# Performance work log

Hardware: AMD Instinct MI355X
Metric: run time of the kernel (lower is better)

The kernel has to match this reference:

```python
import jax, jax.numpy as jnp
import numpy as np

N_POINTS = 16384
N_GAUSS = 3200
N_CLASSES = 14
BOX = 10.0  # scene half-extent


def setup_inputs() -> dict:
    key = jax.random.key(0)
    ks = jax.random.split(key, 6)
    xyz = jax.random.uniform(ks[0], (N_POINTS, 3), jnp.float32, -BOX, BOX)
    means = jax.random.uniform(ks[1], (N_GAUSS, 3), jnp.float32, -BOX, BOX)
    scales = jax.random.uniform(ks[2], (N_GAUSS, 3), jnp.float32, 0.5, 2.0)
    rotations = jax.random.normal(ks[3], (N_GAUSS, 4), jnp.float32)
    opacities = jax.random.uniform(ks[4], (N_GAUSS,), jnp.float32, 0.1, 1.0)
    semantics = jax.random.normal(ks[5], (N_GAUSS, N_CLASSES), jnp.float32)
    return {"xyz": xyz, "means": means, "scales": scales,
            "rotations": rotations, "opacities": opacities, "semantics": semantics}


def quat_to_rot(q):
    # q: [G,4] in (w, x, y, z) order, normalized first (matches torch helper)
    q = q / jnp.linalg.norm(q, axis=-1, keepdims=True)
    w, x, y, z = q[:, 0], q[:, 1], q[:, 2], q[:, 3]
    R = jnp.stack([
        1 - 2 * (y * y + z * z), 2 * (x * y - w * z),     2 * (x * z + w * y),
        2 * (x * y + w * z),     1 - 2 * (x * x + z * z), 2 * (y * z - w * x),
        2 * (x * z - w * y),     2 * (y * z + w * x),     1 - 2 * (x * x + y * y),
    ], axis=-1).reshape(-1, 3, 3)
    return R


def reference(xyz, means, scales, rotations, opacities, semantics):
    # Cov = (S R)^T (S R) = R^T diag(s^2) R ; closed-form inverse (R orthonormal):
    # CovInv = R^T diag(1/s^2) R  -- fused analytic 3x3 inverse.
    R = quat_to_rot(rotations)                      # [G,3,3]
    inv_var = 1.0 / (scales * scales)               # [G,3]
    CovInv = jnp.einsum('gki,gk,gkj->gij', R, inv_var, R)  # [G,3,3]

    # Quadratic form q[n,g] = (x_n - mu_g)^T A_g (x_n - mu_g), expanded so that
    # only [N,G] is materialized (no [N,G,3] intermediates):
    Amu = jnp.einsum('gij,gj->gi', CovInv, means)   # [G,3]
    muAmu = jnp.sum(means * Amu, axis=-1)           # [G]
    P = (xyz[:, :, None] * xyz[:, None, :]).reshape(-1, 9)   # [N,9]
    Aflat = CovInv.reshape(-1, 9)                   # [G,9]
    q = P @ Aflat.T - 2.0 * (xyz @ Amu.T) + muAmu[None, :]   # [N,G]

    # Gaussian splat aggregation: semantics weighted by opacity * Gaussian kernel
    w = opacities[None, :] * jnp.exp(-0.5 * q)      # [N,G]
    out = w @ semantics                              # [N,C]
    return out
```

## Files before the change

### kernel.cpp

```cpp
#include <hip/hip_runtime.h>
#include <hip/hip_bf16.h>

#define N_POINTS 16384
#define N_GAUSS  3200
#define N_CLASSES 14
#define NCHUNK (N_GAUSS / 32)

typedef _Float16 half8  __attribute__((ext_vector_type(8)));
typedef _Float16 half2v __attribute__((ext_vector_type(2)));
typedef float    f32x4  __attribute__((ext_vector_type(4)));

#define WS_CREC_OFF 0
#define WS_SEMP_OFF 204800

__global__ void gauss_prep_kernel(const float* __restrict__ means,
                                  const float* __restrict__ scales,
                                  const float* __restrict__ rotations,
                                  const float* __restrict__ opacities,
                                  const float* __restrict__ semantics,
                                  _Float16* __restrict__ crec,
                                  _Float16* __restrict__ semP,
                                  float* __restrict__ out) {
    const int gid = blockIdx.x * blockDim.x + threadIdx.x;

#pragma unroll
    for (int i = 0; i < N_CLASSES; ++i)
        out[i * N_POINTS + gid] = 0.0f;

    const int g = gid;
    if (g >= N_GAUSS) return;

    float qw = rotations[g * 4 + 0];
    float qx = rotations[g * 4 + 1];
    float qy = rotations[g * 4 + 2];
    float qz = rotations[g * 4 + 3];
    float inv = 1.0f / sqrtf(qw * qw + qx * qx + qy * qy + qz * qz);
    qw *= inv; qx *= inv; qy *= inv; qz *= inv;

    float r00 = 1.0f - 2.0f * (qy * qy + qz * qz);
    float r01 = 2.0f * (qx * qy - qw * qz);
    float r02 = 2.0f * (qx * qz + qw * qy);
    float r10 = 2.0f * (qx * qy + qw * qz);
    float r11 = 1.0f - 2.0f * (qx * qx + qz * qz);
    float r12 = 2.0f * (qy * qz - qw * qx);
    float r20 = 2.0f * (qx * qz - qw * qy);
    float r21 = 2.0f * (qy * qz + qw * qx);
    float r22 = 1.0f - 2.0f * (qx * qx + qy * qy);

    float sx = scales[g * 3 + 0];
    float sy = scales[g * 3 + 1];
    float sz = scales[g * 3 + 2];
    float iv0 = 1.0f / (sx * sx);
    float iv1 = 1.0f / (sy * sy);
    float iv2 = 1.0f / (sz * sz);

    float a00 = iv0 * r00 * r00 + iv1 * r10 * r10 + iv2 * r20 * r20;
    float a01 = iv0 * r00 * r01 + iv1 * r10 * r11 + iv2 * r20 * r21;
    float a02 = iv0 * r00 * r02 + iv1 * r10 * r12 + iv2 * r20 * r22;
    float a11 = iv0 * r01 * r01 + iv1 * r11 * r11 + iv2 * r21 * r21;
    float a12 = iv0 * r01 * r02 + iv1 * r11 * r12 + iv2 * r21 * r22;
    float a22 = iv0 * r02 * r02 + iv1 * r12 * r12 + iv2 * r22 * r22;

    float mx = means[g * 3 + 0];
    float my = means[g * 3 + 1];
    float mz = means[g * 3 + 2];
    float amx = a00 * mx + a01 * my + a02 * mz;
    float amy = a01 * mx + a11 * my + a12 * mz;
    float amz = a02 * mx + a12 * my + a22 * mz;
    float muAmu = mx * amx + my * amy + mz * amz;

    const float k = -0.72134752044448170368f;

    float C[10];
    C[0] = k * a00;  C[1] = k * a11;  C[2] = k * a22;
    C[3] = 2.0f * k * a01;  C[4] = 2.0f * k * a02;  C[5] = 2.0f * k * a12;
    C[6] = -2.0f * k * amx; C[7] = -2.0f * k * amy; C[8] = -2.0f * k * amz;
    C[9] = k * muAmu + log2f(opacities[g]);

    _Float16* rec = crec + (size_t)g * 32;
#pragma unroll
    for (int kk = 0; kk < 10; ++kk) {
        _Float16 h = (_Float16)C[kk];
        rec[kk]      = h;
        rec[10 + kk] = (_Float16)(C[kk] - (float)h);
        rec[20 + kk] = h;
    }
    rec[30] = (_Float16)0; rec[31] = (_Float16)0;

    const int cidx = g >> 5, r = g & 31;
    const int gt = r >> 4, grpW = (r >> 2) & 3, i = r & 3;
    const int p = grpW * 8 + gt * 4 + i;
#pragma unroll
    for (int c = 0; c < N_CLASSES; ++c)
        semP[(size_t)c * N_GAUSS + cidx * 32 + p] = (_Float16)semantics[g * N_CLASSES + c];
}

__launch_bounds__(512, 4)
__global__ void gauss_occ_main_kernel(const float* __restrict__ xyz,
                                      const _Float16* __restrict__ crec,
                                      const _Float16* __restrict__ semP,
                                      float* __restrict__ out) {
    __shared__ unsigned int wbuf[8][64][16];

    const int tid  = threadIdx.x;
    const int lane = tid & 63;
    const int wid  = __builtin_amdgcn_readfirstlane(tid >> 6);
    const int pg    = blockIdx.x >> 2;
    const int split = blockIdx.x & 3;
    const int slot  = split * 8 + wid;
    const int c0 = (slot * NCHUNK) >> 5;
    const int c1 = ((slot + 1) * NCHUNK) >> 5;

    const int m   = lane & 15;
    const int mm  = (m < N_CLASSES) ? m : (N_CLASSES - 1);
    const int grp = lane >> 4;
    const int frs = (m >> 1) & 3;
    const int wsz = (lane >> 1) & 3;

    const int pt = pg * 64 + lane;
    const float x = xyz[pt * 3 + 0];
    const float y = xyz[pt * 3 + 1];
    const float z = xyz[pt * 3 + 2];

    unsigned int (*wrow)[16] = wbuf[wid];

    {
        float P[10] = {x * x, y * y, z * z, x * y, x * z, y * z, x, y, z, 1.0f};
        _Float16 Ph[10], Pl[10];
#pragma unroll
        for (int j = 0; j < 10; ++j) {
            Ph[j] = (_Float16)P[j];
            Pl[j] = (_Float16)(P[j] - (float)Ph[j]);
        }
        half8 b0, b1, b2, b3;
#pragma unroll
        for (int j = 0; j < 8; ++j) b0[j] = Ph[j];
        b1[0] = Ph[8]; b1[1] = Ph[9];
#pragma unroll
        for (int j = 0; j < 6; ++j) b1[2 + j] = Ph[j];
#pragma unroll
        for (int j = 0; j < 4; ++j) { b2[j] = Ph[6 + j]; b2[4 + j] = Pl[j]; }
#pragma unroll
        for (int j = 0; j < 6; ++j) b3[j] = Pl[4 + j];
        b3[6] = (_Float16)0; b3[7] = (_Float16)0;
        *(half8*)&wrow[lane][(0 ^ wsz) * 4] = b0;
        *(half8*)&wrow[lane][(1 ^ wsz) * 4] = b1;
        *(half8*)&wrow[lane][(2 ^ wsz) * 4] = b2;
        *(half8*)&wrow[lane][(3 ^ wsz) * 4] = b3;
    }

    half8 f1[4];
#pragma unroll
    for (int s = 0; s < 4; ++s)
        f1[s] = *(const half8*)&wrow[s * 16 + m][(grp ^ frs) * 4];

    f32x4 acc0 = {0.f, 0.f, 0.f, 0.f};
    f32x4 acc1 = {0.f, 0.f, 0.f, 0.f};
    f32x4 acc2 = {0.f, 0.f, 0.f, 0.f};
    f32x4 acc3 = {0.f, 0.f, 0.f, 0.f};
    const f32x4 z4 = {0.f, 0.f, 0.f, 0.f};

    for (int c = c0; c < c1; ++c) {
        const size_t rbase = ((size_t)(c * 32 + m)) * 32 + grp * 8;
        const half8 A0 = *(const half8*)(crec + rbase);
        const half8 A1 = *(const half8*)(crec + rbase + 16 * 32);
        const half8 bS = *(const half8*)(semP + (size_t)mm * N_GAUSS + c * 32 + grp * 8);

#pragma unroll
        for (int s = 0; s < 4; ++s) {
            f32x4 t0 = __builtin_amdgcn_mfma_f32_16x16x32_f16(A0, f1[s], z4, 0, 0, 0);
            f32x4 t1 = __builtin_amdgcn_mfma_f32_16x16x32_f16(A1, f1[s], z4, 0, 0, 0);

            half2v h01, h23, h45, h67;
            h01[0] = (_Float16)__builtin_amdgcn_exp2f(t0[0]);
            h01[1] = (_Float16)__builtin_amdgcn_exp2f(t0[1]);
            h23[0] = (_Float16)__builtin_amdgcn_exp2f(t0[2]);
            h23[1] = (_Float16)__builtin_amdgcn_exp2f(t0[3]);
            h45[0] = (_Float16)__builtin_amdgcn_exp2f(t1[0]);
            h45[1] = (_Float16)__builtin_amdgcn_exp2f(t1[1]);
            h67[0] = (_Float16)__builtin_amdgcn_exp2f(t1[2]);
            h67[1] = (_Float16)__builtin_amdgcn_exp2f(t1[3]);

            *(uint4*)&wrow[s * 16 + m][(grp ^ frs) * 4] =
                make_uint4(__builtin_bit_cast(unsigned int, h01),
                           __builtin_bit_cast(unsigned int, h23),
                           __builtin_bit_cast(unsigned int, h45),
                           __builtin_bit_cast(unsigned int, h67));
        }

        const half8 a0 = *(const half8*)&wrow[ 0 + m][(grp ^ frs) * 4];
        const half8 a1 = *(const half8*)&wrow[16 + m][(grp ^ frs) * 4];
        const half8 a2 = *(const half8*)&wrow[32 + m][(grp ^ frs) * 4];
        const half8 a3 = *(const half8*)&wrow[48 + m][(grp ^ frs) * 4];
        acc0 = __builtin_amdgcn_mfma_f32_16x16x32_f16(a0, bS, acc0, 0, 0, 0);
        acc1 = __builtin_amdgcn_mfma_f32_16x16x32_f16(a1, bS, acc1, 0, 0, 0);
        acc2 = __builtin_amdgcn_mfma_f32_16x16x32_f16(a2, bS, acc2, 0, 0, 0);
        acc3 = __builtin_amdgcn_mfma_f32_16x16x32_f16(a3, bS, acc3, 0, 0, 0);
    }

    float* red = (float*)&wbuf[0][0][0];
#pragma unroll
    for (int i = 0; i < 4; ++i) {
        red[wid * 1024 + ( 0 + grp * 4 + i) * 16 + m] = acc0[i];
        red[wid * 1024 + (16 + grp * 4 + i) * 16 + m] = acc1[i];
        red[wid * 1024 + (32 + grp * 4 + i) * 16 + m] = acc2[i];
        red[wid * 1024 + (48 + grp * 4 + i) * 16 + m] = acc3[i];
    }
    __syncthreads();

    for (int idx = tid; idx < 64 * N_CLASSES; idx += 512) {
        const int l = idx / N_CLASSES;
        const int cc = idx - l * N_CLASSES;
        float s = 0.0f;
#pragma unroll
        for (int wq = 0; wq < 8; ++wq) s += red[wq * 1024 + l * 16 + cc];
        unsafeAtomicAdd(&out[(pg * 64 + l) * N_CLASSES + cc], s);
    }
}

extern "C" void kernel_launch(void* const* d_in, const int* in_sizes, int n_in,
                              void* d_out, int out_size, void* d_ws, size_t ws_size,
                              hipStream_t stream) {
    const float* xyz       = (const float*)d_in[0];
    const float* means     = (const float*)d_in[1];
    const float* scales    = (const float*)d_in[2];
    const float* rotations = (const float*)d_in[3];
    const float* opacities = (const float*)d_in[4];
    const float* semantics = (const float*)d_in[5];
    float* out = (float*)d_out;

    _Float16* crec = (_Float16*)((char*)d_ws + WS_CREC_OFF);
    _Float16* semP = (_Float16*)((char*)d_ws + WS_SEMP_OFF);

    hipLaunchKernelGGL(gauss_prep_kernel,
                       dim3(64), dim3(256), 0, stream,
                       means, scales, rotations, opacities, semantics, crec, semP, out);

    hipLaunchKernelGGL(gauss_occ_main_kernel,
                       dim3(256 * 4), dim3(512), 0, stream,
                       xyz, crec, semP, out);
}
```

Before: 21.24 us.

## Drop Gaussian split across blocks, write outputs directly, prefetch next chunk

The main kernel now uses one block per 64-point group, with its 8 waves covering all Gaussian chunks, instead of four blocks each covering a quarter of the chunks. Because of this, the block reduction can store results directly, so the output zeroing in the prep kernel and the global atomics are removed. The next chunk's coefficient and semantic fragments are also register-prefetched while the current chunk is being processed. The trade-off is that only 256 blocks are launched, which reduces parallelism on a large GPU, and the longer per-wave loop with prefetch registers may reduce occupancy.

```diff
diff --git a/kernel.cpp b/kernel.cpp
--- a/kernel.cpp
+++ b/kernel.cpp
@@ -19,15 +19,8 @@
                                   const float* __restrict__ opacities,
                                   const float* __restrict__ semantics,
                                   _Float16* __restrict__ crec,
-                                  _Float16* __restrict__ semP,
-                                  float* __restrict__ out) {
-    const int gid = blockIdx.x * blockDim.x + threadIdx.x;
-
-#pragma unroll
-    for (int i = 0; i < N_CLASSES; ++i)
-        out[i * N_POINTS + gid] = 0.0f;
-
-    const int g = gid;
+                                  _Float16* __restrict__ semP) {
+    const int g = blockIdx.x * blockDim.x + threadIdx.x;
     if (g >= N_GAUSS) return;
 
     float qw = rotations[g * 4 + 0];
@@ -95,7 +88,7 @@
         semP[(size_t)c * N_GAUSS + cidx * 32 + p] = (_Float16)semantics[g * N_CLASSES + c];
 }
 
-__launch_bounds__(512, 4)
+__launch_bounds__(512, 2)
 __global__ void gauss_occ_main_kernel(const float* __restrict__ xyz,
                                       const _Float16* __restrict__ crec,
                                       const _Float16* __restrict__ semP,
@@ -105,11 +98,9 @@
     const int tid  = threadIdx.x;
     const int lane = tid & 63;
     const int wid  = __builtin_amdgcn_readfirstlane(tid >> 6);
-    const int pg    = blockIdx.x >> 2;
-    const int split = blockIdx.x & 3;
-    const int slot  = split * 8 + wid;
-    const int c0 = (slot * NCHUNK) >> 5;
-    const int c1 = ((slot + 1) * NCHUNK) >> 5;
+    const int pg   = blockIdx.x;
+    const int c0 = (wid * NCHUNK) >> 3;
+    const int c1 = ((wid + 1) * NCHUNK) >> 3;
 
     const int m   = lane & 15;
     const int mm  = (m < N_CLASSES) ? m : (N_CLASSES - 1);
@@ -160,11 +151,17 @@
     f32x4 acc3 = {0.f, 0.f, 0.f, 0.f};
     const f32x4 z4 = {0.f, 0.f, 0.f, 0.f};
 
+    size_t rb = ((size_t)(c0 * 32 + m)) * 32 + (size_t)grp * 8;
+    half8 A0 = *(const half8*)(crec + rb);
+    half8 A1 = *(const half8*)(crec + rb + 16 * 32);
+    half8 bS = *(const half8*)(semP + (size_t)mm * N_GAUSS + c0 * 32 + grp * 8);
+
     for (int c = c0; c < c1; ++c) {
-        const size_t rbase = ((size_t)(c * 32 + m)) * 32 + grp * 8;
-        const half8 A0 = *(const half8*)(crec + rbase);
-        const half8 A1 = *(const half8*)(crec + rbase + 16 * 32);
-        const half8 bS = *(const half8*)(semP + (size_t)mm * N_GAUSS + c * 32 + grp * 8);
+        const int cn = (c + 1 < c1) ? (c + 1) : c;
+        const size_t rbn = ((size_t)(cn * 32 + m)) * 32 + (size_t)grp * 8;
+        const half8 nA0 = *(const half8*)(crec + rbn);
+        const half8 nA1 = *(const half8*)(crec + rbn + 16 * 32);
+        const half8 nbS = *(const half8*)(semP + (size_t)mm * N_GAUSS + cn * 32 + grp * 8);
 
 #pragma unroll
         for (int s = 0; s < 4; ++s) {
@@ -196,6 +193,8 @@
         acc1 = __builtin_amdgcn_mfma_f32_16x16x32_f16(a1, bS, acc1, 0, 0, 0);
         acc2 = __builtin_amdgcn_mfma_f32_16x16x32_f16(a2, bS, acc2, 0, 0, 0);
         acc3 = __builtin_amdgcn_mfma_f32_16x16x32_f16(a3, bS, acc3, 0, 0, 0);
+
+        A0 = nA0; A1 = nA1; bS = nbS;
     }
 
     float* red = (float*)&wbuf[0][0][0];
@@ -214,7 +213,7 @@
         float s = 0.0f;
 #pragma unroll
         for (int wq = 0; wq < 8; ++wq) s += red[wq * 1024 + l * 16 + cc];
-        unsafeAtomicAdd(&out[(pg * 64 + l) * N_CLASSES + cc], s);
+        out[(size_t)pg * (64 * N_CLASSES) + idx] = s;
     }
 }
 
@@ -233,10 +232,10 @@
     _Float16* semP = (_Float16*)((char*)d_ws + WS_SEMP_OFF);
 
     hipLaunchKernelGGL(gauss_prep_kernel,
-                       dim3(64), dim3(256), 0, stream,
-                       means, scales, rotations, opacities, semantics, crec, semP, out);
+                       dim3(13), dim3(256), 0, stream,
+                       means, scales, rotations, opacities, semantics, crec, semP);
 
     hipLaunchKernelGGL(gauss_occ_main_kernel,
-                       dim3(256 * 4), dim3(512), 0, stream,
+                       dim3(256), dim3(512), 0, stream,
                        xyz, crec, semP, out);
 }
```

New measurement: 19.45 us. 8.4% less time.
